# Kernel tuning notes

Measured on AMD Instinct MI355X. Metric: run time of the kernel, lower is better.

The kernel has to match this reference:

```python
import jax, jax.numpy as jnp
import numpy as np

D_MODEL = 1024
NUM_HEADS = 16
HEAD_DIM = D_MODEL // NUM_HEADS


def setup_inputs() -> dict:
    key = jax.random.key(0)
    k_x, k_qw, k_qb, k_ow, k_ob = jax.random.split(key, 5)
    s = 1.0 / np.sqrt(D_MODEL)
    return {
        "x": jax.random.normal(k_x, (2, 2048, D_MODEL), dtype=jnp.float32),
        "qkv_w": jax.random.uniform(k_qw, (3 * D_MODEL, D_MODEL), jnp.float32, -s, s),
        "qkv_b": jax.random.uniform(k_qb, (3 * D_MODEL,), jnp.float32, -s, s),
        "out_w": jax.random.uniform(k_ow, (D_MODEL, D_MODEL), jnp.float32, -s, s),
        "out_b": jax.random.uniform(k_ob, (D_MODEL,), jnp.float32, -s, s),
    }


def reference(x, qkv_w, qkv_b, out_w, out_b):
    B, S, D = x.shape
    # fused QKV projection: [B,S,3D]
    qkv = jnp.einsum("bsd,ed->bse", x, qkv_w) + qkv_b
    # [B,S,H,3*hd] -> [B,H,S,3*hd]
    qkv = qkv.reshape(B, S, NUM_HEADS, 3 * HEAD_DIM).transpose(0, 2, 1, 3)
    q, k, v = jnp.split(qkv, 3, axis=-1)
    scale = 1.0 / jnp.sqrt(jnp.asarray(HEAD_DIM, x.dtype))
    scores = jnp.einsum("bhqd,bhkd->bhqk", q, k) * scale
    attn = jax.nn.softmax(scores, axis=-1)
    vals = jnp.einsum("bhqk,bhkd->bhqd", attn, v)
    vals = vals.transpose(0, 2, 1, 3).reshape(B, S, D)
    return jnp.einsum("bsd,ed->bse", vals, out_w) + out_b
```

## Files before the change

kernel.cpp:

```cpp
#include <hip/hip_runtime.h>
#include <stdint.h>


#define D_MODEL 1024
#define NUM_HEADS 16
#define HEAD_DIM 64
#define BATCH 2
#define SEQ 2048
#define M_TOT (BATCH * SEQ)
#define QKV_N (3 * D_MODEL)

typedef __attribute__((ext_vector_type(8))) short bf16x8;
typedef __attribute__((ext_vector_type(4))) short bf16x4;
typedef __attribute__((ext_vector_type(4))) float f32x4;
typedef __attribute__((ext_vector_type(4))) unsigned int u32x4;

#if __has_builtin(__builtin_amdgcn_exp2f)
#define EXP2(x) __builtin_amdgcn_exp2f(x)
#else
#define EXP2(x) exp2f(x)
#endif

__device__ __forceinline__ unsigned short f2bf(float f) {
    union { float f; unsigned int u; } v; v.f = f;
    unsigned int u = v.u;
    u += 0x7fffu + ((u >> 16) & 1u);
    return (unsigned short)(u >> 16);
}

__device__ __forceinline__ unsigned int pack_bf16_rhu(float lo, float hi) {
    union { float f; unsigned int u; } a, b;
    a.f = lo; b.f = hi;
#if __has_builtin(__builtin_amdgcn_perm)
    return __builtin_amdgcn_perm(b.u + 0x8000u, a.u + 0x8000u, 0x07060302u);
#else
    return ((b.u + 0x8000u) & 0xFFFF0000u) | ((a.u + 0x8000u) >> 16);
#endif
}

__device__ __forceinline__ void gld_lds16(const unsigned short* g,
                                          unsigned short* l) {
#if __has_builtin(__builtin_amdgcn_global_load_lds)
    __builtin_amdgcn_global_load_lds(
        (const __attribute__((address_space(1))) unsigned int*)g,
        (__attribute__((address_space(3))) unsigned int*)l, 16, 0, 0);
#else
    *(u32x4*)(l + (threadIdx.x & 63) * 8) = *(const u32x4*)g;
#endif
}

__global__ __launch_bounds__(256) void cvt_f32_bf16(const float* __restrict__ src,
                                                    unsigned short* __restrict__ dst,
                                                    int n8) {
    int i = blockIdx.x * 256 + threadIdx.x;
    if (i >= n8) return;
    const float4* s = (const float4*)src;
    float4 a = s[2 * i], b = s[2 * i + 1];
    u32x4 o;
    o.x = (unsigned int)f2bf(a.x) | ((unsigned int)f2bf(a.y) << 16);
    o.y = (unsigned int)f2bf(a.z) | ((unsigned int)f2bf(a.w) << 16);
    o.z = (unsigned int)f2bf(b.x) | ((unsigned int)f2bf(b.y) << 16);
    o.w = (unsigned int)f2bf(b.z) | ((unsigned int)f2bf(b.w) << 16);
    *(u32x4*)(dst + 8 * (size_t)i) = o;
}

__device__ __forceinline__ void gemm_tile(const unsigned short* __restrict__ A,
                                          const unsigned short* __restrict__ Bw,
                                          int K, int m0, int n0,
                                          unsigned short* As, unsigned short* Bs,
                                          f32x4 acc[4][4]) {
    const int tid = threadIdx.x;
    const int lane = tid & 63;
    const int wave = tid >> 6;
    const int wm = (wave >> 1) * 64;
    const int wn = (wave & 1) * 64;
    const int quad = lane >> 4;
    const int l16 = lane & 15;
    const int lrow = lane >> 3;
    const int sw = (lane & 7) ^ (lrow & 7);
    const int l7 = l16 & 7;

#pragma unroll
    for (int mt = 0; mt < 4; mt++)
#pragma unroll
        for (int nt = 0; nt < 4; nt++) acc[mt][nt] = (f32x4)0.0f;

    for (int kt = 0; kt < K; kt += 64) {
#pragma unroll
        for (int i = 0; i < 4; ++i) {
            int R = wave * 32 + i * 8;
            int grow = R + lrow;
            gld_lds16(A + (size_t)(m0 + grow) * K + kt + sw * 8, As + R * 64);
            gld_lds16(Bw + (size_t)(n0 + grow) * K + kt + sw * 8, Bs + R * 64);
        }
        __syncthreads();
#pragma unroll
        for (int ks = 0; ks < 2; ++ks) {
            int cxl = ((ks * 4 + quad) ^ l7) * 8;
            bf16x8 af[4], bf[4];
#pragma unroll
            for (int mt = 0; mt < 4; mt++)
                af[mt] = *(const bf16x8*)(As + (wm + mt * 16 + l16) * 64 + cxl);
#pragma unroll
            for (int nt = 0; nt < 4; nt++)
                bf[nt] = *(const bf16x8*)(Bs + (wn + nt * 16 + l16) * 64 + cxl);
#pragma unroll
            for (int mt = 0; mt < 4; mt++)
#pragma unroll
                for (int nt = 0; nt < 4; nt++)
                    acc[mt][nt] = __builtin_amdgcn_mfma_f32_16x16x32_bf16(
                        af[mt], bf[nt], acc[mt][nt], 0, 0, 0);
        }
        __syncthreads();
    }
}

__global__ __launch_bounds__(256) void gemm_qkv(const unsigned short* __restrict__ xb,
                                                const unsigned short* __restrict__ wb,
                                                const float* __restrict__ bias,
                                                unsigned short* __restrict__ qb,
                                                unsigned short* __restrict__ kb,
                                                unsigned short* __restrict__ vtb) {
    __shared__ __align__(16) unsigned short As[128 * 64];
    __shared__ __align__(16) unsigned short Bs[128 * 64];
    f32x4 acc[4][4];
    const int m0 = blockIdx.y * 128, n0 = blockIdx.x * 128;
    gemm_tile(xb, wb, D_MODEL, m0, n0, As, Bs, acc);

    const int tid = threadIdx.x;
    const int lane = tid & 63, wave = tid >> 6;
    const int wm = (wave >> 1) * 64, wn = (wave & 1) * 64;
    const int quad = lane >> 4, l16 = lane & 15;
    const float QSCALE = 0.18033688011112042f;
#pragma unroll
    for (int mt = 0; mt < 4; mt++) {
#pragma unroll
        for (int nt = 0; nt < 4; nt++) {
            int e = n0 + wn + nt * 16 + l16;
            float bia = bias[e];
            int h = e / 192;
            int j = e - h * 192;
#pragma unroll
            for (int r = 0; r < 4; r++) {
                int m = m0 + wm + mt * 16 + quad * 4 + r;
                int b = m >> 11;
                int s = m & 2047;
                float v = acc[mt][nt][r] + bia;
                size_t bh = (size_t)(b * NUM_HEADS + h);
                if (j < 64)
                    qb[(bh * SEQ + s) * 64 + j] = f2bf(v * QSCALE);
                else if (j < 128)
                    kb[(bh * SEQ + s) * 64 + (j - 64)] = f2bf(v);
                else
                    vtb[(bh * 64 + (j - 128)) * SEQ + s] = f2bf(v);
            }
        }
    }
}

__global__ __launch_bounds__(256) void attn(const unsigned short* __restrict__ qb,
                                            const unsigned short* __restrict__ kb,
                                            const unsigned short* __restrict__ vtb,
                                            unsigned short* __restrict__ vals) {
    __shared__ __align__(16) unsigned short Ks[2][64 * 64];
    __shared__ __align__(16) unsigned short VTs[2][64 * 64];

    const int tid = threadIdx.x;
    const int lane = tid & 63, wave = tid >> 6;
    const int quad = lane >> 4, l16 = lane & 15;
    const int l7 = l16 & 7;
    const int bh = blockIdx.x;
    const int q0 = blockIdx.y * 128;
    const unsigned short* qh = qb + (size_t)bh * SEQ * 64;
    const unsigned short* kh = kb + (size_t)bh * SEQ * 64;
    const unsigned short* vth = vtb + (size_t)bh * 64 * SEQ;
    const int wrow = wave * 32;

    bf16x8 aq[2][2];
#pragma unroll
    for (int nq = 0; nq < 2; nq++)
#pragma unroll
        for (int ks = 0; ks < 2; ++ks)
            aq[nq][ks] = *(const bf16x8*)(
                qh + (size_t)(q0 + wrow + nq * 16 + l16) * 64 + ks * 32 + quad * 8);

    const int lrow = lane >> 3;
    const int sw = (lane & 7) ^ (lrow & 7);

    auto stage = [&](int t, int b) {
        int kt = t * 64;
#pragma unroll
        for (int i = 0; i < 2; ++i) {
            int R = wave * 16 + i * 8;
            int row = R + lrow;
            gld_lds16(kh + (size_t)(kt + row) * 64 + sw * 8, &Ks[b][R * 64]);
            gld_lds16(vth + (size_t)row * SEQ + kt + sw * 8, &VTs[b][R * 64]);
        }
    };

    stage(0, 0);
    __syncthreads();

    f32x4 oacc[2][4];
    f32x4 lsum[2];
#pragma unroll
    for (int mt = 0; mt < 2; mt++) {
        lsum[mt] = (f32x4)0.0f;
#pragma unroll
        for (int nt = 0; nt < 4; nt++) oacc[mt][nt] = (f32x4)0.0f;
    }

    bf16x4 ones4;
#pragma unroll
    for (int j = 0; j < 4; j++) ones4[j] = (short)0x3F80;

    const int NT = SEQ / 64;
    for (int t = 0; t < NT; ++t) {
        const int cur = t & 1;
        if (t + 1 < NT) stage(t + 1, cur ^ 1);
        const unsigned short* Kc = Ks[cur];
        const unsigned short* Vc = VTs[cur];

        f32x4 sacc[4][2];
#pragma unroll
        for (int mk = 0; mk < 4; mk++)
#pragma unroll
            for (int nq = 0; nq < 2; nq++) sacc[mk][nq] = (f32x4)0.0f;
#pragma unroll
        for (int ks = 0; ks < 2; ++ks) {
            int cxl = ((ks * 4 + quad) ^ l7) * 8;
            bf16x8 bk[4];
#pragma unroll
            for (int mk = 0; mk < 4; mk++)
                bk[mk] = *(const bf16x8*)(Kc + (mk * 16 + l16) * 64 + cxl);
#pragma unroll
            for (int mk = 0; mk < 4; mk++)
#pragma unroll
                for (int nq = 0; nq < 2; nq++)
                    sacc[mk][nq] = __builtin_amdgcn_mfma_f32_16x16x32_bf16(
                        bk[mk], aq[nq][ks], sacc[mk][nq], 0, 0, 0);
        }

        bf16x4 pf[4][2];
#pragma unroll
        for (int mk = 0; mk < 4; mk++)
#pragma unroll
            for (int nq = 0; nq < 2; nq++) {
                float e0 = EXP2(sacc[mk][nq][0]), e1 = EXP2(sacc[mk][nq][1]);
                float e2 = EXP2(sacc[mk][nq][2]), e3 = EXP2(sacc[mk][nq][3]);
                union { unsigned int u[2]; bf16x4 b; } cv;
                cv.u[0] = pack_bf16_rhu(e0, e1);
                cv.u[1] = pack_bf16_rhu(e2, e3);
                pf[mk][nq] = cv.b;
            }

#pragma unroll
        for (int kbk = 0; kbk < 4; ++kbk) {
            int vxl = ((kbk * 2 + (quad >> 1)) ^ l7) * 8 + (quad & 1) * 4;
            bf16x4 bv[4];
#pragma unroll
            for (int nt = 0; nt < 4; nt++)
                bv[nt] = *(const bf16x4*)(Vc + (nt * 16 + l16) * 64 + vxl);
#pragma unroll
            for (int mt = 0; mt < 2; mt++) {
#pragma unroll
                for (int nt = 0; nt < 4; nt++)
                    oacc[mt][nt] = __builtin_amdgcn_mfma_f32_16x16x16bf16_1k(
                        pf[kbk][mt], bv[nt], oacc[mt][nt], 0, 0, 0);
                lsum[mt] = __builtin_amdgcn_mfma_f32_16x16x16bf16_1k(
                    pf[kbk][mt], ones4, lsum[mt], 0, 0, 0);
            }
        }
        __syncthreads();
    }

    const int b = bh >> 4, h = bh & 15;
#pragma unroll
    for (int mt = 0; mt < 2; mt++) {
        f32x4 inv;
#pragma unroll
        for (int r = 0; r < 4; r++) inv[r] = 1.0f / lsum[mt][r];
#pragma unroll
        for (int nt = 0; nt < 4; nt++) {
            int d = nt * 16 + l16;
#pragma unroll
            for (int r = 0; r < 4; r++) {
                int row = wrow + mt * 16 + quad * 4 + r;
                float v = oacc[mt][nt][r] * inv[r];
                vals[((size_t)(b * SEQ + q0 + row)) * D_MODEL + h * 64 + d] =
                    f2bf(v);
            }
        }
    }
}

__global__ __launch_bounds__(256) void gemm_out(const unsigned short* __restrict__ vb,
                                                const unsigned short* __restrict__ wb,
                                                const float* __restrict__ bias,
                                                float* __restrict__ out) {
    __shared__ __align__(16) unsigned short As[128 * 64];
    __shared__ __align__(16) unsigned short Bs[128 * 64];
    f32x4 acc[4][4];
    const int m0 = blockIdx.y * 128, n0 = blockIdx.x * 128;
    gemm_tile(vb, wb, D_MODEL, m0, n0, As, Bs, acc);

    const int tid = threadIdx.x;
    const int lane = tid & 63, wave = tid >> 6;
    const int wm = (wave >> 1) * 64, wn = (wave & 1) * 64;
    const int quad = lane >> 4, l16 = lane & 15;
#pragma unroll
    for (int mt = 0; mt < 4; mt++) {
#pragma unroll
        for (int nt = 0; nt < 4; nt++) {
            int n = n0 + wn + nt * 16 + l16;
            float bia = bias[n];
#pragma unroll
            for (int r = 0; r < 4; r++) {
                int m = m0 + wm + mt * 16 + quad * 4 + r;
                out[(size_t)m * D_MODEL + n] = acc[mt][nt][r] + bia;
            }
        }
    }
}

extern "C" void kernel_launch(void* const* d_in, const int* in_sizes, int n_in,
                              void* d_out, int out_size, void* d_ws, size_t ws_size,
                              hipStream_t stream) {
    const float* x = (const float*)d_in[0];
    const float* qkv_w = (const float*)d_in[1];
    const float* qkv_b = (const float*)d_in[2];
    const float* out_w = (const float*)d_in[3];
    const float* out_b = (const float*)d_in[4];
    float* out = (float*)d_out;

    char* ws = (char*)d_ws;
    size_t off = 0;
    auto carve = [&](size_t bytes) -> void* {
        void* p = ws + off;
        off += (bytes + 255) & ~(size_t)255;
        return p;
    };
    unsigned short* xb  = (unsigned short*)carve((size_t)M_TOT * D_MODEL * 2);
    unsigned short* wqb = (unsigned short*)carve((size_t)QKV_N * D_MODEL * 2);
    unsigned short* wob = (unsigned short*)carve((size_t)D_MODEL * D_MODEL * 2);
    unsigned short* qbuf = (unsigned short*)carve((size_t)M_TOT * D_MODEL * 2);
    unsigned short* kbuf = (unsigned short*)carve((size_t)M_TOT * D_MODEL * 2);
    unsigned short* vtb  = (unsigned short*)carve((size_t)M_TOT * D_MODEL * 2);
    unsigned short* vals = xb;

    int n8x = M_TOT * D_MODEL / 8;
    int n8q = QKV_N * D_MODEL / 8;
    int n8o = D_MODEL * D_MODEL / 8;
    cvt_f32_bf16<<<(n8x + 255) / 256, 256, 0, stream>>>(x, xb, n8x);
    cvt_f32_bf16<<<(n8q + 255) / 256, 256, 0, stream>>>(qkv_w, wqb, n8q);
    cvt_f32_bf16<<<(n8o + 255) / 256, 256, 0, stream>>>(out_w, wob, n8o);

    gemm_qkv<<<dim3(QKV_N / 128, M_TOT / 128), 256, 0, stream>>>(
        xb, wqb, qkv_b, qbuf, kbuf, vtb);

    attn<<<dim3(BATCH * NUM_HEADS, SEQ / 128), 256, 0, stream>>>(
        qbuf, kbuf, vtb, vals);

    gemm_out<<<dim3(D_MODEL / 128, M_TOT / 128), 256, 0, stream>>>(
        vals, wob, out_b, out);
}
```

Before: 213.2 us.

## Stage QKV epilogue through LDS, fuse conversions, approximate exp2, retile output GEMM

The three fp32-to-bf16 conversion launches become a single kernel. The QKV GEMM epilogue now writes its tile to swizzled LDS and stores it back as coalesced 16-byte chunks, including the transposed V layout, replacing scattered 2-byte stores. In attention, exp2 is replaced by a bit trick (fma then float-to-int) that builds the bf16 pattern directly, trading accuracy for fewer transcendental ops. The output GEMM uses 128x64 tiles to double the block count, without double buffering.

```diff
diff --git a/kernel.cpp b/kernel.cpp
--- a/kernel.cpp
+++ b/kernel.cpp
@@ -15,12 +15,6 @@
 typedef __attribute__((ext_vector_type(4))) float f32x4;
 typedef __attribute__((ext_vector_type(4))) unsigned int u32x4;
 
-#if __has_builtin(__builtin_amdgcn_exp2f)
-#define EXP2(x) __builtin_amdgcn_exp2f(x)
-#else
-#define EXP2(x) exp2f(x)
-#endif
-
 __device__ __forceinline__ unsigned short f2bf(float f) {
     union { float f; unsigned int u; } v; v.f = f;
     unsigned int u = v.u;
@@ -28,13 +22,15 @@
     return (unsigned short)(u >> 16);
 }
 
-__device__ __forceinline__ unsigned int pack_bf16_rhu(float lo, float hi) {
-    union { float f; unsigned int u; } a, b;
-    a.f = lo; b.f = hi;
+__device__ __forceinline__ unsigned int exp2_bf16u(float x) {
+    return (unsigned int)__builtin_fmaf(x, 128.0f, 16251.58f);
+}
+
+__device__ __forceinline__ unsigned int perm_pack(unsigned int hi, unsigned int lo) {
 #if __has_builtin(__builtin_amdgcn_perm)
-    return __builtin_amdgcn_perm(b.u + 0x8000u, a.u + 0x8000u, 0x07060302u);
+    return __builtin_amdgcn_perm(hi, lo, 0x05040100u);
 #else
-    return ((b.u + 0x8000u) & 0xFFFF0000u) | ((a.u + 0x8000u) >> 16);
+    return (lo & 0xFFFFu) | (hi << 16);
 #endif
 }
 
@@ -49,19 +45,27 @@
 #endif
 }
 
-__global__ __launch_bounds__(256) void cvt_f32_bf16(const float* __restrict__ src,
-                                                    unsigned short* __restrict__ dst,
-                                                    int n8) {
+__global__ __launch_bounds__(256) void cvt_all(const float* __restrict__ x,
+                                               const float* __restrict__ qw,
+                                               const float* __restrict__ ow,
+                                               unsigned short* __restrict__ xb,
+                                               unsigned short* __restrict__ wqb,
+                                               unsigned short* __restrict__ wob) {
     int i = blockIdx.x * 256 + threadIdx.x;
-    if (i >= n8) return;
+    const int N1 = M_TOT * D_MODEL / 8;
+    const int N2 = N1 + QKV_N * D_MODEL / 8;
+    const float* src; unsigned short* dst; int j;
+    if (i < N1)      { src = x;  dst = xb;  j = i; }
+    else if (i < N2) { src = qw; dst = wqb; j = i - N1; }
+    else             { src = ow; dst = wob; j = i - N2; }
     const float4* s = (const float4*)src;
-    float4 a = s[2 * i], b = s[2 * i + 1];
+    float4 a = s[2 * j], b = s[2 * j + 1];
     u32x4 o;
     o.x = (unsigned int)f2bf(a.x) | ((unsigned int)f2bf(a.y) << 16);
     o.y = (unsigned int)f2bf(a.z) | ((unsigned int)f2bf(a.w) << 16);
     o.z = (unsigned int)f2bf(b.x) | ((unsigned int)f2bf(b.y) << 16);
     o.w = (unsigned int)f2bf(b.z) | ((unsigned int)f2bf(b.w) << 16);
-    *(u32x4*)(dst + 8 * (size_t)i) = o;
+    *(u32x4*)(dst + 8 * (size_t)j) = o;
 }
 
 __device__ __forceinline__ void gemm_tile(const unsigned short* __restrict__ A,
@@ -132,28 +136,60 @@
     const int wm = (wave >> 1) * 64, wn = (wave & 1) * 64;
     const int quad = lane >> 4, l16 = lane & 15;
     const float QSCALE = 0.18033688011112042f;
-#pragma unroll
-    for (int mt = 0; mt < 4; mt++) {
+
+    const int s64 = (n0 + wn) >> 6;
+    const int h = s64 / 3;
+    const int sec = s64 - h * 3;
+    const int bh = (m0 >> 11) * NUM_HEADS + h;
+    const int sbase = (m0 + wm) & 2047;
+
+    unsigned short* sm = ((wave & 2) ? Bs : As) + (wave & 1) * 4096;
+
+    if (sec < 2) {
+        const float scl = (sec == 0) ? QSCALE : 1.0f;
 #pragma unroll
         for (int nt = 0; nt < 4; nt++) {
-            int e = n0 + wn + nt * 16 + l16;
-            float bia = bias[e];
-            int h = e / 192;
-            int j = e - h * 192;
-#pragma unroll
-            for (int r = 0; r < 4; r++) {
-                int m = m0 + wm + mt * 16 + quad * 4 + r;
-                int b = m >> 11;
-                int s = m & 2047;
-                float v = acc[mt][nt][r] + bia;
-                size_t bh = (size_t)(b * NUM_HEADS + h);
-                if (j < 64)
-                    qb[(bh * SEQ + s) * 64 + j] = f2bf(v * QSCALE);
-                else if (j < 128)
-                    kb[(bh * SEQ + s) * 64 + (j - 64)] = f2bf(v);
-                else
-                    vtb[(bh * 64 + (j - 128)) * SEQ + s] = f2bf(v);
+            int c = nt * 16 + l16;
+            float bia = bias[n0 + wn + c];
+#pragma unroll
+            for (int mt = 0; mt < 4; mt++)
+#pragma unroll
+                for (int r = 0; r < 4; r++) {
+                    int row = mt * 16 + quad * 4 + r;
+                    sm[row * 64 + ((((c >> 3) ^ (row & 7)) << 3) | (c & 7))] =
+                        f2bf((acc[mt][nt][r] + bia) * scl);
+                }
+        }
+        unsigned short* dstb = (sec == 0) ? qb : kb;
+#pragma unroll
+        for (int p = 0; p < 8; p++) {
+            int row = p * 8 + (lane >> 3);
+            int g = lane & 7;
+            u32x4 ch = *(const u32x4*)(sm + row * 64 + ((g ^ (row & 7)) << 3));
+            *(u32x4*)(dstb + ((size_t)bh * SEQ + sbase + row) * 64 + g * 8) = ch;
+        }
+    } else {
+#pragma unroll
+        for (int nt = 0; nt < 4; nt++) {
+            int d = nt * 16 + l16;
+            float bia = bias[n0 + wn + d];
+#pragma unroll
+            for (int mt = 0; mt < 4; mt++) {
+                int c = mt * 16 + quad * 4;
+                unsigned short t4[4];
+#pragma unroll
+                for (int r = 0; r < 4; r++) t4[r] = f2bf(acc[mt][nt][r] + bia);
+                *(uint64_t*)(sm + d * 64 +
+                             ((((c >> 3) ^ (d & 7)) << 3) | (c & 7))) =
+                    *(const uint64_t*)t4;
             }
+        }
+#pragma unroll
+        for (int p = 0; p < 8; p++) {
+            int row = p * 8 + (lane >> 3);
+            int g = lane & 7;
+            u32x4 ch = *(const u32x4*)(sm + row * 64 + ((g ^ (row & 7)) << 3));
+            *(u32x4*)(vtb + ((size_t)bh * 64 + row) * SEQ + sbase + g * 8) = ch;
         }
     }
 }
@@ -246,11 +282,13 @@
         for (int mk = 0; mk < 4; mk++)
 #pragma unroll
             for (int nq = 0; nq < 2; nq++) {
-                float e0 = EXP2(sacc[mk][nq][0]), e1 = EXP2(sacc[mk][nq][1]);
-                float e2 = EXP2(sacc[mk][nq][2]), e3 = EXP2(sacc[mk][nq][3]);
+                unsigned int u0 = exp2_bf16u(sacc[mk][nq][0]);
+                unsigned int u1 = exp2_bf16u(sacc[mk][nq][1]);
+                unsigned int u2 = exp2_bf16u(sacc[mk][nq][2]);
+                unsigned int u3 = exp2_bf16u(sacc[mk][nq][3]);
                 union { unsigned int u[2]; bf16x4 b; } cv;
-                cv.u[0] = pack_bf16_rhu(e0, e1);
-                cv.u[1] = pack_bf16_rhu(e2, e3);
+                cv.u[0] = perm_pack(u1, u0);
+                cv.u[1] = perm_pack(u3, u2);
                 pf[mk][nq] = cv.b;
             }
 
@@ -299,19 +337,60 @@
                                                 const float* __restrict__ bias,
                                                 float* __restrict__ out) {
     __shared__ __align__(16) unsigned short As[128 * 64];
-    __shared__ __align__(16) unsigned short Bs[128 * 64];
-    f32x4 acc[4][4];
-    const int m0 = blockIdx.y * 128, n0 = blockIdx.x * 128;
-    gemm_tile(vb, wb, D_MODEL, m0, n0, As, Bs, acc);
-
+    __shared__ __align__(16) unsigned short Bs[64 * 64];
     const int tid = threadIdx.x;
     const int lane = tid & 63, wave = tid >> 6;
-    const int wm = (wave >> 1) * 64, wn = (wave & 1) * 64;
+    const int wm = (wave >> 1) * 64, wn = (wave & 1) * 32;
     const int quad = lane >> 4, l16 = lane & 15;
-#pragma unroll
-    for (int mt = 0; mt < 4; mt++) {
-#pragma unroll
-        for (int nt = 0; nt < 4; nt++) {
+    const int lrow = lane >> 3;
+    const int sw = (lane & 7) ^ (lrow & 7);
+    const int l7 = l16 & 7;
+    const int m0 = blockIdx.y * 128, n0 = blockIdx.x * 64;
+
+    f32x4 acc[4][2];
+#pragma unroll
+    for (int mt = 0; mt < 4; mt++)
+#pragma unroll
+        for (int nt = 0; nt < 2; nt++) acc[mt][nt] = (f32x4)0.0f;
+
+    for (int kt = 0; kt < D_MODEL; kt += 64) {
+#pragma unroll
+        for (int i = 0; i < 4; ++i) {
+            int R = wave * 32 + i * 8;
+            gld_lds16(vb + (size_t)(m0 + R + lrow) * D_MODEL + kt + sw * 8,
+                      As + R * 64);
+        }
+#pragma unroll
+        for (int i = 0; i < 2; ++i) {
+            int R = wave * 16 + i * 8;
+            gld_lds16(wb + (size_t)(n0 + R + lrow) * D_MODEL + kt + sw * 8,
+                      Bs + R * 64);
+        }
+        __syncthreads();
+#pragma unroll
+        for (int ks = 0; ks < 2; ++ks) {
+            int cxl = ((ks * 4 + quad) ^ l7) * 8;
+            bf16x8 af[4], bf[2];
+#pragma unroll
+            for (int mt = 0; mt < 4; mt++)
+                af[mt] = *(const bf16x8*)(As + (wm + mt * 16 + l16) * 64 + cxl);
+#pragma unroll
+            for (int nt = 0; nt < 2; nt++)
+                bf[nt] = *(const bf16x8*)(Bs + (wn + nt * 16 + l16) * 64 + cxl);
+#pragma unroll
+            for (int mt = 0; mt < 4; mt++)
+#pragma unroll
+                for (int nt = 0; nt < 2; nt++)
+                    acc[mt][nt] = __builtin_amdgcn_mfma_f32_16x16x32_bf16(
+                        af[mt], bf[nt], acc[mt][nt], 0, 0, 0);
+        }
+        __syncthreads();
+    }
+
+#pragma unroll
+    for (int mt = 0; mt < 4; mt++)
+#pragma unroll
+        for (int nt = 0; nt < 2; nt++) {
             int n = n0 + wn + nt * 16 + l16;
             float bia = bias[n];
 #pragma unroll
@@ -320,7 +399,6 @@
                 out[(size_t)m * D_MODEL + n] = acc[mt][nt][r] + bia;
             }
         }
-    }
 }
 
 extern "C" void kernel_launch(void* const* d_in, const int* in_sizes, int n_in,
@@ -348,12 +426,8 @@
     unsigned short* vtb  = (unsigned short*)carve((size_t)M_TOT * D_MODEL * 2);
     unsigned short* vals = xb;
 
-    int n8x = M_TOT * D_MODEL / 8;
-    int n8q = QKV_N * D_MODEL / 8;
-    int n8o = D_MODEL * D_MODEL / 8;
-    cvt_f32_bf16<<<(n8x + 255) / 256, 256, 0, stream>>>(x, xb, n8x);
-    cvt_f32_bf16<<<(n8q + 255) / 256, 256, 0, stream>>>(qkv_w, wqb, n8q);
-    cvt_f32_bf16<<<(n8o + 255) / 256, 256, 0, stream>>>(out_w, wob, n8o);
+    const int NCHUNK = (M_TOT + QKV_N + D_MODEL) * D_MODEL / 8;
+    cvt_all<<<NCHUNK / 256, 256, 0, stream>>>(x, qkv_w, out_w, xb, wqb, wob);
 
     gemm_qkv<<<dim3(QKV_N / 128, M_TOT / 128), 256, 0, stream>>>(
         xb, wqb, qkv_b, qbuf, kbuf, vtb);
@@ -361,6 +435,6 @@
     attn<<<dim3(BATCH * NUM_HEADS, SEQ / 128), 256, 0, stream>>>(
         qbuf, kbuf, vtb, vals);
 
-    gemm_out<<<dim3(D_MODEL / 128, M_TOT / 128), 256, 0, stream>>>(
+    gemm_out<<<dim3(D_MODEL / 64, M_TOT / 128), 256, 0, stream>>>(
         vals, wob, out_b, out);
 }
```

Result: faster. 189.5 us (-11.1%).
